# Performance work log

Measured on AMD Instinct MI355X. Metric: run time of the kernel, lower is better.

The kernel has to match this reference:

```python
import jax, jax.numpy as jnp
import numpy as np

B, N, D = 4, 4096, 128
LOSS_WEIGHT = 1.0  # module hardcodes self.loss_weight = 1.0


def setup_inputs() -> dict:
    key = jax.random.key(0)
    k1, k2 = jax.random.split(key)
    corr_pred = jax.random.normal(k1, (B, N, D), dtype=jnp.float32)
    corr_target = jax.random.normal(k2, (B, N, D), dtype=jnp.float32)
    return {"corr_pred": corr_pred, "corr_target": corr_target}


def chamfer_distance(x, y):
    # x: [B, N, D], y: [B, N, D]
    x2 = jnp.sum(x * x, axis=-1)                      # [B, N]  diag of x @ x^T
    y2 = jnp.sum(y * y, axis=-1)                      # [B, N]  diag of y @ y^T
    zz = jnp.einsum('bnd,bmd->bnm', x, y)             # [B, N, N]
    # P[b,i,j] = ||x_i||^2 + ||y_j||^2 - 2 x_i . y_j
    P = x2[:, :, None] + y2[:, None, :] - 2.0 * zz
    P = jnp.clip(P, 0.0, 100.0)
    return jnp.mean(jnp.min(P, axis=1)) + jnp.mean(jnp.min(P, axis=2))


def reference(corr_pred, corr_target):
    chamfer = chamfer_distance(corr_pred, corr_target)
    return LOSS_WEIGHT * chamfer / corr_target.shape[0]
```

## Files before the change

kernel.cpp:

```cpp
#include <hip/hip_runtime.h>
#include <hip/hip_bf16.h>

#define B_ 4
#define N_ 4096
#define D_ 128
#define EPB (N_ * D_)
#define COFF 1024.0f

typedef float f32x4 __attribute__((ext_vector_type(4)));
typedef float f32x2 __attribute__((ext_vector_type(2)));
typedef int   int8v __attribute__((ext_vector_type(8)));
typedef int   int4v __attribute__((ext_vector_type(4)));

#define SQRT2 1.41421356237309515f


__global__ __launch_bounds__(256) void prep_kernel(
    const float* __restrict__ X, const float* __restrict__ Y,
    unsigned char* __restrict__ Xb, unsigned char* __restrict__ Yb,
    float* __restrict__ x2, float* __restrict__ y2,
    int* __restrict__ rowmin, int* __restrict__ colmin)
{
    const int which = blockIdx.y;
    const float* __restrict__ src = which ? Y : X;
    unsigned char* __restrict__ dst = which ? Yb : Xb;
    float* __restrict__ nrm = which ? y2 : x2;
    int* __restrict__ mn = which ? colmin : rowmin;

    const int t = threadIdx.x;
    const int r = t >> 4, c = t & 15;
    const int rgG = blockIdx.x;
    const int row = rgG * 16 + r;

    const float4 v0 = *(const float4*)(src + (size_t)row * D_ + c * 8);
    const float4 v1 = *(const float4*)(src + (size_t)row * D_ + c * 8 + 4);

    float sq = v0.x * v0.x;
    sq = fmaf(v0.y, v0.y, sq); sq = fmaf(v0.z, v0.z, sq); sq = fmaf(v0.w, v0.w, sq);
    sq = fmaf(v1.x, v1.x, sq); sq = fmaf(v1.y, v1.y, sq);
    sq = fmaf(v1.z, v1.z, sq); sq = fmaf(v1.w, v1.w, sq);
    #pragma unroll
    for (int m = 1; m < 16; m <<= 1) sq += __shfl_xor(sq, m);

    unsigned lo = 0, hi = 0;
    lo = __builtin_amdgcn_cvt_pk_fp8_f32(v0.x * SQRT2, v0.y * SQRT2, lo, false);
    lo = __builtin_amdgcn_cvt_pk_fp8_f32(v0.z * SQRT2, v0.w * SQRT2, lo, true);
    hi = __builtin_amdgcn_cvt_pk_fp8_f32(v1.x * SQRT2, v1.y * SQRT2, hi, false);
    hi = __builtin_amdgcn_cvt_pk_fp8_f32(v1.z * SQRT2, v1.w * SQRT2, hi, true);

    const int b = row >> 12;
    const int rg = (row & (N_ - 1)) >> 4;
    uint2 packed; packed.x = lo; packed.y = hi;
    *(uint2*)(dst + (size_t)b * EPB + rg * 2048 + (c >> 2) * 512
              + r * 32 + (c & 3) * 8) = packed;

    if (c == 0) {
        nrm[row] = sq;
        mn[row] = 0x7f7fffff;
    }
}

__global__ __launch_bounds__(256, 2) void chamfer_mfma(
    const unsigned char* __restrict__ Xb, const unsigned char* __restrict__ Yb,
    const float* __restrict__ x2, const float* __restrict__ y2,
    int* __restrict__ rowmin, int* __restrict__ colmin)
{
    const int b = blockIdx.z;
    const int iT = blockIdx.y;
    const int jc = blockIdx.x;
    const int tid = threadIdx.x;
    const int wave = tid >> 6, lane = tid & 63;
    const int quad = lane >> 4, l16 = lane & 15;
    const int rowBase = iT * 256 + wave * 64;

    const unsigned char* __restrict__ Xp = Xb + (size_t)b * EPB;
    const unsigned char* __restrict__ Yp = Yb + (size_t)b * EPB;

    int8v af[4];
    #pragma unroll
    for (int rt = 0; rt < 4; rt++) {
        const unsigned char* ap = Xp + ((rowBase >> 4) + rt) * 2048
                                 + quad * 512 + l16 * 32;
        const int4v lo = *(const int4v*)(ap);
        const int4v hi = *(const int4v*)(ap + 16);
        af[rt] = (int8v){lo.x, lo.y, lo.z, lo.w, hi.x, hi.y, hi.z, hi.w};
    }
    float x2v[4][4];
    #pragma unroll
    for (int rt = 0; rt < 4; rt++)
        #pragma unroll
        for (int i = 0; i < 4; i++)
            x2v[rt][i] = x2[(size_t)b * N_ + rowBase + rt * 16 + quad * 4 + i];

    float rmin[4][4];
    #pragma unroll
    for (int rt = 0; rt < 4; rt++)
        #pragma unroll
        for (int i = 0; i < 4; i++) rmin[rt][i] = 3.0e38f;

    for (int s = 0; s < 4; ++s) {
        const int colBase = jc * 256 + s * 64;
        const int cg = colBase >> 4;

        float y2v[4];
        #pragma unroll
        for (int ct = 0; ct < 4; ct++)
            y2v[ct] = y2[(size_t)b * N_ + colBase + ct * 16 + l16];

        int8v bfv[4];
        #pragma unroll
        for (int ct = 0; ct < 4; ct++) {
            const unsigned char* bp = Yp + (size_t)(cg + ct) * 2048
                                     + quad * 512 + l16 * 32;
            const int4v lo = *(const int4v*)(bp);
            const int4v hi = *(const int4v*)(bp + 16);
            bfv[ct] = (int8v){lo.x, lo.y, lo.z, lo.w, hi.x, hi.y, hi.z, hi.w};
        }

        #pragma unroll
        for (int h = 0; h < 2; ++h) {
            f32x4 acc[4][2];
            #pragma unroll
            for (int i = 0; i < 4; i++)
                #pragma unroll
                for (int j = 0; j < 2; j++)
                    acc[i][j] = (f32x4){0.f, 0.f, 0.f, 0.f};

            #pragma unroll
            for (int rt = 0; rt < 4; rt++)
                #pragma unroll
                for (int c2 = 0; c2 < 2; c2++)
                    acc[rt][c2] = __builtin_amdgcn_mfma_scale_f32_16x16x128_f8f6f4(
                        af[rt], bfv[h * 2 + c2], acc[rt][c2],
                        0, 0,
                        0, 127,
                        0, 127);

            float cmin[2];
            #pragma unroll
            for (int c2 = 0; c2 < 2; c2++) cmin[c2] = 3.0e38f;
            #pragma unroll
            for (int rt = 0; rt < 4; rt++)
                #pragma unroll
                for (int i = 0; i < 4; i++) {
                    const float xv = x2v[rt][i];
                    float rm = rmin[rt][i];
                    #pragma unroll
                    for (int c2 = 0; c2 < 2; c2++) {
                        const float a = acc[rt][c2][i];
                        rm = fminf(rm, y2v[h * 2 + c2] - a);
                        cmin[c2] = fminf(cmin[c2], xv - a);
                    }
                    rmin[rt][i] = rm;
                }
            #pragma unroll
            for (int c2 = 0; c2 < 2; c2++) {
                float v = cmin[c2];
                v = fminf(v, __shfl_xor(v, 16));
                v = fminf(v, __shfl_xor(v, 32));
                if (quad == 0)
                    atomicMin(&colmin[(size_t)b * N_ + colBase
                                      + (h * 2 + c2) * 16 + l16],
                              __float_as_int(v + COFF));
            }
        }
    }

    #pragma unroll
    for (int rt = 0; rt < 4; rt++)
        #pragma unroll
        for (int i = 0; i < 4; i++) {
            float v = rmin[rt][i];
            #pragma unroll
            for (int m = 1; m < 16; m <<= 1) v = fminf(v, __shfl_xor(v, m));
            if (l16 == 0) {
                float c = fminf(fmaxf(x2v[rt][i] + v, 0.0f), 100.0f);
                atomicMin(&rowmin[(size_t)b * N_ + rowBase + rt * 16 + quad * 4 + i],
                          __float_as_int(c));
            }
        }
}

__global__ __launch_bounds__(256) void finalize1_kernel(
    const int* __restrict__ rowmin, const int* __restrict__ colmin,
    const float* __restrict__ y2, float* __restrict__ partial)
{
    const int i = blockIdx.x * 256 + threadIdx.x;
    float s;
    {
        int4 v = ((const int4*)rowmin)[i];
        s  = __int_as_float(v.x) + __int_as_float(v.y) +
             __int_as_float(v.z) + __int_as_float(v.w);
        int4 c = ((const int4*)colmin)[i];
        float4 yv = ((const float4*)y2)[i];
        s += fminf(fmaxf(__int_as_float(c.x) - COFF + yv.x, 0.f), 100.f);
        s += fminf(fmaxf(__int_as_float(c.y) - COFF + yv.y, 0.f), 100.f);
        s += fminf(fmaxf(__int_as_float(c.z) - COFF + yv.z, 0.f), 100.f);
        s += fminf(fmaxf(__int_as_float(c.w) - COFF + yv.w, 0.f), 100.f);
    }
    #pragma unroll
    for (int m = 1; m < 64; m <<= 1) s += __shfl_xor(s, m);
    __shared__ float sm[4];
    if ((threadIdx.x & 63) == 0) sm[threadIdx.x >> 6] = s;
    __syncthreads();
    if (threadIdx.x == 0)
        partial[blockIdx.x] = sm[0] + sm[1] + sm[2] + sm[3];
}

__global__ __launch_bounds__(64) void finalize2_kernel(
    const float* __restrict__ partial, float* __restrict__ out)
{
    const int l = threadIdx.x;
    float s = (l < 16) ? partial[l] : 0.f;
    #pragma unroll
    for (int m = 1; m < 16; m <<= 1) s += __shfl_xor(s, m);
    if (l == 0)
        out[0] = s / ((float)B_ * (float)N_) / (float)B_;
}

extern "C" void kernel_launch(void* const* d_in, const int* in_sizes, int n_in,
                              void* d_out, int out_size, void* d_ws, size_t ws_size,
                              hipStream_t stream) {
    const float* X = (const float*)d_in[0];
    const float* Y = (const float*)d_in[1];

    char* ws = (char*)d_ws;
    const size_t f8_bytes = (size_t)B_ * N_ * D_;
    unsigned char* Xb = (unsigned char*)ws;
    unsigned char* Yb = (unsigned char*)(ws + f8_bytes);
    char* ws2 = ws + 2 * f8_bytes;
    const size_t vec_bytes = (size_t)B_ * N_ * 4;
    float* x2      = (float*)(ws2);
    float* y2      = (float*)(ws2 + vec_bytes);
    int*   rowmin  = (int*)  (ws2 + 2 * vec_bytes);
    int*   colmin  = (int*)  (ws2 + 3 * vec_bytes);
    float* partial = (float*)(ws2 + 4 * vec_bytes);
    float* out = (float*)d_out;

    prep_kernel<<<dim3(B_ * N_ / 16, 2), 256, 0, stream>>>(
        X, Y, Xb, Yb, x2, y2, rowmin, colmin);
    chamfer_mfma<<<dim3(16, N_ / 256, B_), 256, 0, stream>>>(
        Xb, Yb, x2, y2, rowmin, colmin);
    finalize1_kernel<<<16, 256, 0, stream>>>(rowmin, colmin, y2, partial);
    finalize2_kernel<<<1, 64, 0, stream>>>(partial, out);
}
```

Baseline: 90.92 us.

## Double-buffer Y fragment loads across 32-column steps in chamfer MFMA loop

Splits the column loop into 32-column steps and loads the next step's fp8 Y fragments and y2 norms into a second register set while the current step's MFMAs and min reductions run. The goal is to hide global-load latency behind compute instead of stalling at the start of each 64-column chunk. The x2 norms are now read with a single vector load. Two buffer sets raise register pressure, which could hurt occupancy under launch_bounds(256,2).

```diff
diff --git a/kernel.cpp b/kernel.cpp
--- a/kernel.cpp
+++ b/kernel.cpp
@@ -8,7 +8,6 @@
 #define COFF 1024.0f
 
 typedef float f32x4 __attribute__((ext_vector_type(4)));
-typedef float f32x2 __attribute__((ext_vector_type(2)));
 typedef int   int8v __attribute__((ext_vector_type(8)));
 typedef int   int4v __attribute__((ext_vector_type(4)));
 
@@ -59,6 +58,61 @@
         mn[row] = 0x7f7fffff;
     }
 }
+
+
+#define PREF(B0, B1, Y0, Y1, H) do {                                          \
+    const int cb_ = jc * 256 + (H) * 32;                                      \
+    const unsigned char* bp0_ = Yp + (size_t)(cb_ >> 4) * 2048                \
+                               + quad * 512 + l16 * 32;                       \
+    const int4v lo0_ = *(const int4v*)(bp0_);                                 \
+    const int4v hi0_ = *(const int4v*)(bp0_ + 16);                            \
+    const int4v lo1_ = *(const int4v*)(bp0_ + 2048);                          \
+    const int4v hi1_ = *(const int4v*)(bp0_ + 2064);                          \
+    B0 = (int8v){lo0_.x, lo0_.y, lo0_.z, lo0_.w, hi0_.x, hi0_.y, hi0_.z, hi0_.w}; \
+    B1 = (int8v){lo1_.x, lo1_.y, lo1_.z, lo1_.w, hi1_.x, hi1_.y, hi1_.z, hi1_.w}; \
+    Y0 = y2[(size_t)b * N_ + cb_ + l16];                                      \
+    Y1 = y2[(size_t)b * N_ + cb_ + 16 + l16];                                 \
+} while (0)
+
+#define STEP(B0, B1, Y0, Y1, H) do {                                          \
+    f32x4 acc0_[4], acc1_[4];                                                 \
+    _Pragma("unroll")                                                         \
+    for (int rt = 0; rt < 4; rt++) {                                          \
+        acc0_[rt] = (f32x4){0.f, 0.f, 0.f, 0.f};                              \
+        acc1_[rt] = (f32x4){0.f, 0.f, 0.f, 0.f};                              \
+    }                                                                         \
+    _Pragma("unroll")                                                         \
+    for (int rt = 0; rt < 4; rt++) {                                          \
+        acc0_[rt] = __builtin_amdgcn_mfma_scale_f32_16x16x128_f8f6f4(         \
+            af[rt], B0, acc0_[rt], 0, 0, 0, 127, 0, 127);                     \
+        acc1_[rt] = __builtin_amdgcn_mfma_scale_f32_16x16x128_f8f6f4(         \
+            af[rt], B1, acc1_[rt], 0, 0, 0, 127, 0, 127);                     \
+    }                                                                         \
+    float cm0_ = 3.0e38f, cm1_ = 3.0e38f;                                     \
+    _Pragma("unroll")                                                         \
+    for (int rt = 0; rt < 4; rt++)                                            \
+    _Pragma("unroll")                                                         \
+    for (int i = 0; i < 4; i++) {                                             \
+        const float xv_ = x2v[rt][i];                                         \
+        const float a0_ = acc0_[rt][i], a1_ = acc1_[rt][i];                   \
+        rmin[rt][i] = fminf(rmin[rt][i], fminf(Y0 - a0_, Y1 - a1_));          \
+        cm0_ = fminf(cm0_, xv_ - a0_);                                        \
+        cm1_ = fminf(cm1_, xv_ - a1_);                                        \
+    }                                                                         \
+    {                                                                         \
+        const int cb_ = jc * 256 + (H) * 32;                                  \
+        float v0_ = fminf(cm0_, __shfl_xor(cm0_, 16));                        \
+        v0_ = fminf(v0_, __shfl_xor(v0_, 32));                                \
+        float v1_ = fminf(cm1_, __shfl_xor(cm1_, 16));                        \
+        v1_ = fminf(v1_, __shfl_xor(v1_, 32));                                \
+        if (quad == 0) {                                                      \
+            atomicMin(&colmin[(size_t)b * N_ + cb_ + l16],                    \
+                      __float_as_int(v0_ + COFF));                            \
+            atomicMin(&colmin[(size_t)b * N_ + cb_ + 16 + l16],               \
+                      __float_as_int(v1_ + COFF));                            \
+        }                                                                     \
+    }                                                                         \
+} while (0)
 
 __global__ __launch_bounds__(256, 2) void chamfer_mfma(
     const unsigned char* __restrict__ Xb, const unsigned char* __restrict__ Yb,
@@ -85,12 +139,10 @@
         const int4v hi = *(const int4v*)(ap + 16);
         af[rt] = (int8v){lo.x, lo.y, lo.z, lo.w, hi.x, hi.y, hi.z, hi.w};
     }
-    float x2v[4][4];
+    f32x4 x2v[4];
     #pragma unroll
     for (int rt = 0; rt < 4; rt++)
-        #pragma unroll
-        for (int i = 0; i < 4; i++)
-            x2v[rt][i] = x2[(size_t)b * N_ + rowBase + rt * 16 + quad * 4 + i];
+        x2v[rt] = *(const f32x4*)(x2 + (size_t)b * N_ + rowBase + rt * 16 + quad * 4);
 
     float rmin[4][4];
     #pragma unroll
@@ -98,72 +150,18 @@
         #pragma unroll
         for (int i = 0; i < 4; i++) rmin[rt][i] = 3.0e38f;
 
-    for (int s = 0; s < 4; ++s) {
-        const int colBase = jc * 256 + s * 64;
-        const int cg = colBase >> 4;
-
-        float y2v[4];
-        #pragma unroll
-        for (int ct = 0; ct < 4; ct++)
-            y2v[ct] = y2[(size_t)b * N_ + colBase + ct * 16 + l16];
-
-        int8v bfv[4];
-        #pragma unroll
-        for (int ct = 0; ct < 4; ct++) {
-            const unsigned char* bp = Yp + (size_t)(cg + ct) * 2048
-                                     + quad * 512 + l16 * 32;
-            const int4v lo = *(const int4v*)(bp);
-            const int4v hi = *(const int4v*)(bp + 16);
-            bfv[ct] = (int8v){lo.x, lo.y, lo.z, lo.w, hi.x, hi.y, hi.z, hi.w};
-        }
-
-        #pragma unroll
-        for (int h = 0; h < 2; ++h) {
-            f32x4 acc[4][2];
-            #pragma unroll
-            for (int i = 0; i < 4; i++)
-                #pragma unroll
-                for (int j = 0; j < 2; j++)
-                    acc[i][j] = (f32x4){0.f, 0.f, 0.f, 0.f};
-
-            #pragma unroll
-            for (int rt = 0; rt < 4; rt++)
-                #pragma unroll
-                for (int c2 = 0; c2 < 2; c2++)
-                    acc[rt][c2] = __builtin_amdgcn_mfma_scale_f32_16x16x128_f8f6f4(
-                        af[rt], bfv[h * 2 + c2], acc[rt][c2],
-                        0, 0,
-                        0, 127,
-                        0, 127);
-
-            float cmin[2];
-            #pragma unroll
-            for (int c2 = 0; c2 < 2; c2++) cmin[c2] = 3.0e38f;
-            #pragma unroll
-            for (int rt = 0; rt < 4; rt++)
-                #pragma unroll
-                for (int i = 0; i < 4; i++) {
-                    const float xv = x2v[rt][i];
-                    float rm = rmin[rt][i];
-                    #pragma unroll
-                    for (int c2 = 0; c2 < 2; c2++) {
-                        const float a = acc[rt][c2][i];
-                        rm = fminf(rm, y2v[h * 2 + c2] - a);
-                        cmin[c2] = fminf(cmin[c2], xv - a);
-                    }
-                    rmin[rt][i] = rm;
-                }
-            #pragma unroll
-            for (int c2 = 0; c2 < 2; c2++) {
-                float v = cmin[c2];
-                v = fminf(v, __shfl_xor(v, 16));
-                v = fminf(v, __shfl_xor(v, 32));
-                if (quad == 0)
-                    atomicMin(&colmin[(size_t)b * N_ + colBase
-                                      + (h * 2 + c2) * 16 + l16],
-                              __float_as_int(v + COFF));
-            }
-        }
+    int8v bA0, bA1, bB0, bB1;
+    float yA0, yA1, yB0, yB1;
+    PREF(bA0, bA1, yA0, yA1, 0);
+
+    #pragma clang loop unroll(disable)
+    for (int sp = 0; sp < 4; ++sp) {
+        const int h0 = sp * 2;
+        PREF(bB0, bB1, yB0, yB1, h0 + 1);
+        STEP(bA0, bA1, yA0, yA1, h0);
+        if (sp < 3)
+            PREF(bA0, bA1, yA0, yA1, h0 + 2);
+        STEP(bB0, bB1, yB0, yB1, h0 + 1);
     }
 
     #pragma unroll
```

Result: no change. 91.38 us (+0.5%).
